# Kernel tuning notes

Hardware: AMD Instinct MI355X
Metric: run time of the kernel (lower is better)

The kernel has to match this reference:

```python
import jax, jax.numpy as jnp
import numpy as np

N = 100000   # total nodes
E = 1000000  # edges
D = 64       # input_dim
H = 128      # embed_dim


def setup_inputs() -> dict:
    key = jax.random.key(0)
    k1, k2, k3, k4 = jax.random.split(key, 4)
    nodes = jnp.arange(N, dtype=jnp.int32)
    features = jax.random.normal(k1, (N, D), dtype=jnp.float32)
    edge_index = jax.random.randint(k2, (2, E), 0, N, dtype=jnp.int32)
    # nn.Linear(2*D, H): weight [H, 2D], bias [H]
    W = jax.random.normal(k3, (H, 2 * D), dtype=jnp.float32) / np.sqrt(2 * D)
    b = jax.random.normal(k4, (H,), dtype=jnp.float32) * 0.01
    return {"nodes": nodes, "features": features, "edge_index": edge_index,
            "W": W, "b": b}


def reference(nodes, features, edge_index, W, b):
    src, dst = edge_index[0], edge_index[1]
    # gcn=False: neighbors are undirected (both src->dst and dst->src).
    # Mean aggregator over all neighbors (full-neighborhood mean).
    ones = jnp.ones((E,), dtype=features.dtype)
    neigh_sum = (jax.ops.segment_sum(features[dst], src, num_segments=N)
                 + jax.ops.segment_sum(features[src], dst, num_segments=N))
    deg = (jax.ops.segment_sum(ones, src, num_segments=N)
           + jax.ops.segment_sum(ones, dst, num_segments=N))
    neigh_mean = neigh_sum / jnp.maximum(deg, 1.0)[:, None]  # [N, D]
    self_feats = features[nodes]            # [B, D]
    neigh_feats = neigh_mean[nodes]         # [B, D]
    combined = jnp.concatenate([self_feats, neigh_feats], axis=1)  # [B, 2D]
    out = jax.nn.relu(combined @ W.T + b)   # [B, H]
    return out
```

## Files before the change

### kernel.cpp

```cpp
#include <hip/hip_runtime.h>
#include <hip/hip_bf16.h>


#define D_IN 64
#define H_OUT 128
#define CAP 64
#define CAP_L 61
#define NPB 32
#define BSHIFT 8
#define BUK_N 256
#define NBUK_MAX 512
#define PASSA_BLOCKS 256
#define PASSA_THREADS 512

typedef unsigned long long ull;
typedef unsigned short ushortt;
typedef unsigned char uchar;
typedef __attribute__((ext_vector_type(8))) short bf16x8;
typedef __attribute__((ext_vector_type(4))) float f32x4;
typedef __attribute__((ext_vector_type(2))) float f32x2;

__device__ __forceinline__ ushortt f2bf(float f) {
    __hip_bfloat16 h = __float2bfloat16(f);
    return *reinterpret_cast<ushortt*>(&h);
}
__device__ __forceinline__ float bf2f(ushortt u) {
    unsigned int x = ((unsigned int)u) << 16;
    return __uint_as_float(x);
}

__global__ __launch_bounds__(PASSA_THREADS) void prep_kernel(
    const int* __restrict__ ei,
    unsigned* __restrict__ gbuf,
    int* __restrict__ blkcnt,
    const float4* __restrict__ feat4,
    const float4* __restrict__ w4,
    ushortt* __restrict__ fb,
    uint2* __restrict__ fq,
    ushortt* __restrict__ Wb,
    int E, int nbuk, int scap, int chunk, int nfeat8, int nw8)
{
    const int t = threadIdx.x;

    if (blockIdx.x >= PASSA_BLOCKS) {
        int i = (blockIdx.x - PASSA_BLOCKS) * PASSA_THREADS + t;
        if (i < nfeat8) {
            float4 a = feat4[2 * i], b = feat4[2 * i + 1];
            bf16x8 o;
            o[0] = (short)f2bf(a.x); o[1] = (short)f2bf(a.y);
            o[2] = (short)f2bf(a.z); o[3] = (short)f2bf(a.w);
            o[4] = (short)f2bf(b.x); o[5] = (short)f2bf(b.y);
            o[6] = (short)f2bf(b.z); o[7] = (short)f2bf(b.w);
            *(bf16x8*)&fb[(size_t)i * 8] = o;
            unsigned lo = (unsigned)__builtin_amdgcn_cvt_pk_fp8_f32(a.x, a.y, 0, false);
            lo = (unsigned)__builtin_amdgcn_cvt_pk_fp8_f32(a.z, a.w, (int)lo, true);
            unsigned hi = (unsigned)__builtin_amdgcn_cvt_pk_fp8_f32(b.x, b.y, 0, false);
            hi = (unsigned)__builtin_amdgcn_cvt_pk_fp8_f32(b.z, b.w, (int)hi, true);
            uint2 q; q.x = lo; q.y = hi;
            fq[i] = q;
        } else {
            int j = i - nfeat8;
            if (j < nw8) {
                float4 a = w4[2 * j], b = w4[2 * j + 1];
                bf16x8 o;
                o[0] = (short)f2bf(a.x); o[1] = (short)f2bf(a.y);
                o[2] = (short)f2bf(a.z); o[3] = (short)f2bf(a.w);
                o[4] = (short)f2bf(b.x); o[5] = (short)f2bf(b.y);
                o[6] = (short)f2bf(b.z); o[7] = (short)f2bf(b.w);
                *(bf16x8*)&Wb[(size_t)j * 8] = o;
            }
        }
        return;
    }

    __shared__ int lcnt[NBUK_MAX];
    for (int i = t; i < nbuk; i += PASSA_THREADS) lcnt[i] = 0;
    __syncthreads();

    const int E2 = 2 * E;
    int lo = blockIdx.x * chunk;
    int hi = lo + chunk; if (hi > E2) hi = E2;

    for (int i = lo + t; i < hi; i += PASSA_THREADS) {
        int u = ei[i];
        int v = (i < E) ? ei[E + i] : ei[i - E];
        int b = u >> BSHIFT;
        unsigned pk = ((unsigned)v << BSHIFT) | (unsigned)(u & (BUK_N - 1));
        int p = atomicAdd(&lcnt[b], 1);
        if (p < scap) gbuf[((size_t)blockIdx.x * nbuk + b) * scap + p] = pk;
    }
    __syncthreads();
    for (int b = t; b < nbuk; b += PASSA_THREADS)
        blkcnt[blockIdx.x * nbuk + b] = lcnt[b];
}

__global__ __launch_bounds__(1024) void adj_agg_kernel(
    const unsigned* __restrict__ gbuf,
    const int* __restrict__ blkcnt,
    const int* __restrict__ ei,
    const uchar* __restrict__ fq,
    ushortt* __restrict__ meanb,
    int N, int E, int nbuk, int scap)
{
    __shared__ unsigned adj_l[BUK_N * CAP_L];
    __shared__ int cnt_l[BUK_N];
    __shared__ int scnt_l[PASSA_BLOCKS];
    __shared__ int satf;

    const int b = blockIdx.x;
    const int t = threadIdx.x;

    if (t == 0) satf = 0;
    if (t < BUK_N) cnt_l[t] = 0;
    if (t < PASSA_BLOCKS) {
        int c = blkcnt[t * nbuk + b];
        scnt_l[t] = c;
        if (c > scap) satf = 1;
    }
    __syncthreads();

    const int wv   = t >> 6;
    const int lane = t & 63;

    if (satf) {
        const int E2 = 2 * E;
        for (int i = t; i < E2; i += 1024) {
            int u = ei[i];
            if ((u >> BSHIFT) != b) continue;
            int v = (i < E) ? ei[E + i] : ei[i - E];
            int ul = u & (BUK_N - 1);
            int p  = atomicAdd(&cnt_l[ul], 1);
            if (p < CAP_L) adj_l[ul * CAP_L + p] = (unsigned)v;
        }
    } else {
        for (int seg = wv; seg < PASSA_BLOCKS; seg += 16) {
            int c = scnt_l[seg]; if (c > scap) c = scap;
            const unsigned* base = gbuf + ((size_t)seg * nbuk + b) * scap;
            for (int i = lane; i < c; i += 64) {
                unsigned e = base[i];
                int ul = e & (BUK_N - 1);
                int v  = (int)(e >> BSHIFT);
                int p  = atomicAdd(&cnt_l[ul], 1);
                if (p < CAP_L) adj_l[ul * CAP_L + p] = (unsigned)v;
            }
        }
    }
    __syncthreads();

    const int oct = lane >> 3;
    const int ol  = lane & 7;
    const uchar* fqb = fq + ol * 8;

    const int nbase = wv * 16;
    const int gbase = (b << BSHIFT) + nbase;

#define GATH(U0, U1, U2, U3, AROW, CC)                                       \
    {                                                                        \
        if ((CC) > 0) {                                                      \
            int jj = oct;      int a = jj < (CC);                            \
            unsigned id = (AROW)[a ? jj : 0];                                \
            U0 = *(const uint2*)(fqb + (size_t)(id * 64u));                  \
            if (!a) { U0.x = 0u; U0.y = 0u; }                                \
        }                                                                    \
        if ((CC) > 8) {                                                      \
            int jj = 8 + oct;  int a = jj < (CC);                            \
            unsigned id = (AROW)[a ? jj : 0];                                \
            U1 = *(const uint2*)(fqb + (size_t)(id * 64u));                  \
            if (!a) { U1.x = 0u; U1.y = 0u; }                                \
        }                                                                    \
        if ((CC) > 16) {                                                     \
            int jj = 16 + oct; int a = jj < (CC);                            \
            unsigned id = (AROW)[a ? jj : 0];                                \
            U2 = *(const uint2*)(fqb + (size_t)(id * 64u));                  \
            if (!a) { U2.x = 0u; U2.y = 0u; }                                \
        }                                                                    \
        if ((CC) > 24) {                                                     \
            int jj = 24 + oct; int a = jj < (CC);                            \
            unsigned id = (AROW)[a ? jj : 0];                                \
            U3 = *(const uint2*)(fqb + (size_t)(id * 64u));                  \
            if (!a) { U3.x = 0u; U3.y = 0u; }                                \
        }                                                                    \
    }

#define DEC(u)                                                       \
    s0 += __builtin_amdgcn_cvt_pk_f32_fp8((int)(u).x, false);        \
    s1 += __builtin_amdgcn_cvt_pk_f32_fp8((int)(u).x, true);         \
    s2 += __builtin_amdgcn_cvt_pk_f32_fp8((int)(u).y, false);        \
    s3 += __builtin_amdgcn_cvt_pk_f32_fp8((int)(u).y, true);

#define FINISH(UA, UB, UC, UD, CC, CTRUE, AROW, G)                           \
    {                                                                        \
        f32x2 s0 = {0.f, 0.f}, s1 = {0.f, 0.f};                              \
        f32x2 s2 = {0.f, 0.f}, s3 = {0.f, 0.f};                              \
        DEC(UA); DEC(UB); DEC(UC); DEC(UD);                                  \
        if (__builtin_expect((CC) > 32, 0)) {                                \
            for (int j = 32; j < (CC); j += 8) {                             \
                int jj = j + oct; int a = jj < (CC);                         \
                unsigned id = (AROW)[a ? jj : 0];                            \
                uint2 u = *(const uint2*)(fqb + (size_t)(id * 64u));         \
                if (!a) { u.x = 0u; u.y = 0u; }                              \
                DEC(u);                                                      \
            }                                                                \
        }                                                                    \
        f32x2 a0, a1;                                                        \
        {                                                                    \
            f32x2 t0, t1, t2, t3;                                            \
            t0.x = __shfl_xor(s0.x, 8);  t0.y = __shfl_xor(s0.y, 8);         \
            t1.x = __shfl_xor(s1.x, 8);  t1.y = __shfl_xor(s1.y, 8);         \
            t2.x = __shfl_xor(s2.x, 8);  t2.y = __shfl_xor(s2.y, 8);         \
            t3.x = __shfl_xor(s3.x, 8);  t3.y = __shfl_xor(s3.y, 8);         \
            bool hi = (oct & 1);                                             \
            a0 = hi ? (s2 + t2) : (s0 + t0);                                 \
            a1 = hi ? (s3 + t3) : (s1 + t1);                                 \
        }                                                                    \
        f32x2 b0;                                                            \
        {                                                                    \
            f32x2 t0, t1;                                                    \
            t0.x = __shfl_xor(a0.x, 16); t0.y = __shfl_xor(a0.y, 16);        \
            t1.x = __shfl_xor(a1.x, 16); t1.y = __shfl_xor(a1.y, 16);        \
            bool hi = (oct & 2);                                             \
            b0 = hi ? (a1 + t1) : (a0 + t0);                                 \
        }                                                                    \
        float cf;                                                            \
        {                                                                    \
            f32x2 tt;                                                        \
            tt.x = __shfl_xor(b0.x, 32); tt.y = __shfl_xor(b0.y, 32);        \
            f32x2 ss = b0 + tt;                                              \
            cf = (oct & 4) ? ss.y : ss.x;                                    \
        }                                                                    \
        float r = 1.0f / fmaxf((float)(CTRUE), 1.0f);                        \
        int d = 8 * ol + 4 * (oct & 1) + (oct & 2) + ((oct >> 2) & 1);       \
        meanb[(size_t)(G) * D_IN + d] = f2bf(cf * r);                        \
    }

    for (int np = 0; np < 8; ++np) {
        const int n0 = nbase + 2 * np;
        const int g0 = gbase + 2 * np;
        const int g1 = g0 + 1;

        const int c0  = (g0 < N) ? cnt_l[n0] : 0;
        const int c1  = (g1 < N) ? cnt_l[n0 + 1] : 0;
        const int cc0 = c0 < CAP_L ? c0 : CAP_L;
        const int cc1 = c1 < CAP_L ? c1 : CAP_L;
        const unsigned* ar0 = &adj_l[n0 * CAP_L];
        const unsigned* ar1 = &adj_l[(n0 + 1) * CAP_L];

        uint2 u00 = {0u,0u}, u01 = {0u,0u}, u02 = {0u,0u}, u03 = {0u,0u};
        uint2 u10 = {0u,0u}, u11 = {0u,0u}, u12 = {0u,0u}, u13 = {0u,0u};
        GATH(u00, u01, u02, u03, ar0, cc0);
        GATH(u10, u11, u12, u13, ar1, cc1);

        if (g0 < N) FINISH(u00, u01, u02, u03, cc0, c0, ar0, g0);
        if (g1 < N) FINISH(u10, u11, u12, u13, cc1, c1, ar1, g1);
    }
#undef GATH
#undef DEC
#undef FINISH
}

__global__ __launch_bounds__(256) void build_adj_kernel(
    const int* __restrict__ ei,
    int* __restrict__ cnt,
    int* __restrict__ adj,
    int E)
{
    const int part   = blockIdx.x & 7;
    const int bloc   = blockIdx.x >> 3;
    const int nbp    = gridDim.x >> 3;
    const int stride = nbp * 256;
    const int E2     = 2 * E;

    for (int i = bloc * 256 + (int)threadIdx.x; i < E2; i += stride) {
        int u = ei[i];
        if (((u >> 4) & 7) != part) continue;
        int v = (i < E) ? ei[E + i] : ei[i - E];
        int p = atomicAdd(&cnt[u], 1);
        if (p < CAP_L) adj[u * CAP + p] = v;
    }
}

__global__ __launch_bounds__(256) void aggregate_f32_kernel(
    const float* __restrict__ feat,
    const int* __restrict__ adj,
    const int* __restrict__ cnt,
    ushortt* __restrict__ meanb,
    int N)
{
    int wid  = (blockIdx.x * blockDim.x + threadIdx.x) >> 6;
    int lane = threadIdx.x & 63;
    if (wid >= N) return;

    int c  = cnt[wid];
    int cc = c < CAP_L ? c : CAP_L;
    int ids = adj[wid * CAP + lane];

    float sum = 0.0f;
    int j = 0;
    for (; j + 8 <= cc; j += 8) {
        int i0 = __shfl(ids, j + 0);
        int i1 = __shfl(ids, j + 1);
        int i2 = __shfl(ids, j + 2);
        int i3 = __shfl(ids, j + 3);
        int i4 = __shfl(ids, j + 4);
        int i5 = __shfl(ids, j + 5);
        int i6 = __shfl(ids, j + 6);
        int i7 = __shfl(ids, j + 7);
        float f0 = feat[i0 * D_IN + lane];
        float f1 = feat[i1 * D_IN + lane];
        float f2 = feat[i2 * D_IN + lane];
        float f3 = feat[i3 * D_IN + lane];
        float f4 = feat[i4 * D_IN + lane];
        float f5 = feat[i5 * D_IN + lane];
        float f6 = feat[i6 * D_IN + lane];
        float f7 = feat[i7 * D_IN + lane];
        sum += ((f0 + f1) + (f2 + f3)) + ((f4 + f5) + (f6 + f7));
    }
    for (; j < cc; ++j)
        sum += feat[__shfl(ids, j) * D_IN + lane];

    float m = sum / fmaxf((float)c, 1.0f);
    meanb[(size_t)wid * D_IN + lane] = f2bf(m);
}

__global__ __launch_bounds__(256) void gemm_mfma_kernel(
    const int* __restrict__ nodes,
    const ushortt* __restrict__ fb,
    const ushortt* __restrict__ meanb,
    const ushortt* __restrict__ Wb,
    const float* __restrict__ bias,
    float* __restrict__ out,
    int N)
{
    __shared__ ushortt w_lds[128 * 136];
    __shared__ int gnode[64];

    const int t  = threadIdx.x;
    const int n0 = blockIdx.x * 64;

    if (t < 64) {
        int idx = n0 + t;
        gnode[t] = nodes[idx < N ? idx : N - 1];
    }
    for (int i = t; i < 128 * 16; i += 256) {
        int row = i >> 4, seg = i & 15;
        *(bf16x8*)&w_lds[row * 136 + seg * 8] =
            *(const bf16x8*)&Wb[row * 128 + seg * 8];
    }
    __syncthreads();

    const int w    = t >> 6;
    const int lane = t & 63;
    const int l15  = lane & 15;
    const int quad = lane >> 4;

    const int g = gnode[w * 16 + l15];
    const bf16x8 a0 = *(const bf16x8*)&fb[(size_t)g * D_IN +  0 + quad * 8];
    const bf16x8 a1 = *(const bf16x8*)&fb[(size_t)g * D_IN + 32 + quad * 8];
    const bf16x8 a2 = *(const bf16x8*)&meanb[(size_t)g * D_IN +  0 + quad * 8];
    const bf16x8 a3 = *(const bf16x8*)&meanb[(size_t)g * D_IN + 32 + quad * 8];

    const int  out_row = n0 + w * 16 + l15;
    const bool valid   = out_row < N;

#pragma unroll
    for (int tile = 0; tile < 8; ++tile) {
        const int h0 = tile * 16;
        const ushortt* wrow = &w_lds[(h0 + l15) * 136];
        bf16x8 b0 = *(const bf16x8*)&wrow[ 0 + quad * 8];
        bf16x8 b1 = *(const bf16x8*)&wrow[32 + quad * 8];
        bf16x8 b2 = *(const bf16x8*)&wrow[64 + quad * 8];
        bf16x8 b3 = *(const bf16x8*)&wrow[96 + quad * 8];

        f32x4 acc = {0.f, 0.f, 0.f, 0.f};
        acc = __builtin_amdgcn_mfma_f32_16x16x32_bf16(b0, a0, acc, 0, 0, 0);
        acc = __builtin_amdgcn_mfma_f32_16x16x32_bf16(b1, a1, acc, 0, 0, 0);
        acc = __builtin_amdgcn_mfma_f32_16x16x32_bf16(b2, a2, acc, 0, 0, 0);
        acc = __builtin_amdgcn_mfma_f32_16x16x32_bf16(b3, a3, acc, 0, 0, 0);

        if (valid) {
            float4 bv = *(const float4*)&bias[h0 + quad * 4];
            float4 o;
            o.x = fmaxf(acc[0] + bv.x, 0.0f);
            o.y = fmaxf(acc[1] + bv.y, 0.0f);
            o.z = fmaxf(acc[2] + bv.z, 0.0f);
            o.w = fmaxf(acc[3] + bv.w, 0.0f);
            *(float4*)&out[(size_t)out_row * H_OUT + h0 + quad * 4] = o;
        }
    }
}

__global__ __launch_bounds__(256) void gemm_kernel(
    const int* __restrict__ nodes,
    const float* __restrict__ feat,
    const ushortt* __restrict__ meanb,
    const float* __restrict__ W,
    const float* __restrict__ bias,
    float* __restrict__ out,
    int N)
{
    __shared__ float w_lds[64 * 132];
    __shared__ float comb_self[NPB * 68];
    __shared__ float comb_mean[NPB * 68];
    __shared__ int   gnode[NPB];

    const int t  = threadIdx.x;
    const int n0 = blockIdx.x * NPB;

    if (t < NPB) {
        int idx = n0 + t;
        if (idx >= N) idx = N - 1;
        gnode[t] = nodes[idx];
    }
    __syncthreads();

    for (int i = t; i < NPB * 64; i += 256) {
        int n = i >> 6, d = i & 63;
        int g = gnode[n];
        comb_self[n * 68 + d] = feat[g * D_IN + d];
        comb_mean[n * 68 + d] = bf2f(meanb[(size_t)g * D_IN + d]);
    }
    for (int i = t; i < H_OUT * 64; i += 256) {
        int h = i >> 6, kk = i & 63;
        w_lds[kk * 132 + h] = W[h * (2 * D_IN) + kk];
    }
    __syncthreads();

    const int tx = t & 31;
    const int ty = t >> 5;
    const int h0 = tx * 4;
    const int nl = ty * 4;

    float acc[4][4];
#pragma unroll
    for (int j = 0; j < 4; j++)
#pragma unroll
        for (int i = 0; i < 4; i++) acc[j][i] = 0.0f;

    for (int kk = 0; kk < 64; kk += 4) {
        float4 wvv[4], cv[4];
#pragma unroll
        for (int i = 0; i < 4; i++)
            wvv[i] = *(const float4*)&w_lds[(kk + i) * 132 + h0];
#pragma unroll
        for (int j = 0; j < 4; j++)
            cv[j] = *(const float4*)&comb_self[(nl + j) * 68 + kk];
#pragma unroll
        for (int j = 0; j < 4; j++) {
            const float* c = (const float*)&cv[j];
#pragma unroll
            for (int i = 0; i < 4; i++) {
                const float* wp = (const float*)&wvv[i];
                acc[j][0] += wp[0] * c[i];
                acc[j][1] += wp[1] * c[i];
                acc[j][2] += wp[2] * c[i];
                acc[j][3] += wp[3] * c[i];
            }
        }
    }
    __syncthreads();

    for (int i = t; i < H_OUT * 64; i += 256) {
        int h = i >> 6, kk = i & 63;
        w_lds[kk * 132 + h] = W[h * (2 * D_IN) + 64 + kk];
    }
    __syncthreads();

    for (int kk = 0; kk < 64; kk += 4) {
        float4 wvv[4], cv[4];
#pragma unroll
        for (int i = 0; i < 4; i++)
            wvv[i] = *(const float4*)&w_lds[(kk + i) * 132 + h0];
#pragma unroll
        for (int j = 0; j < 4; j++)
            cv[j] = *(const float4*)&comb_mean[(nl + j) * 68 + kk];
#pragma unroll
        for (int j = 0; j < 4; j++) {
            const float* c = (const float*)&cv[j];
#pragma unroll
            for (int i = 0; i < 4; i++) {
                const float* wp = (const float*)&wvv[i];
                acc[j][0] += wp[0] * c[i];
                acc[j][1] += wp[1] * c[i];
                acc[j][2] += wp[2] * c[i];
                acc[j][3] += wp[3] * c[i];
            }
        }
    }

    float4 bv = *(const float4*)&bias[h0];
#pragma unroll
    for (int j = 0; j < 4; j++) {
        int n = n0 + nl + j;
        if (n >= N) continue;
        float4 o;
        o.x = fmaxf(acc[j][0] + bv.x, 0.0f);
        o.y = fmaxf(acc[j][1] + bv.y, 0.0f);
        o.z = fmaxf(acc[j][2] + bv.z, 0.0f);
        o.w = fmaxf(acc[j][3] + bv.w, 0.0f);
        *(float4*)&out[(size_t)n * H_OUT + h0] = o;
    }
}

extern "C" void kernel_launch(void* const* d_in, const int* in_sizes, int n_in,
                              void* d_out, int out_size, void* d_ws, size_t ws_size,
                              hipStream_t stream) {
    const int*   nodes = (const int*)d_in[0];
    const float* feat  = (const float*)d_in[1];
    const int*   ei    = (const int*)d_in[2];
    const float* W     = (const float*)d_in[3];
    const float* bias  = (const float*)d_in[4];
    float*       out   = (float*)d_out;

    const int N  = in_sizes[0];
    const int E  = in_sizes[2] / 2;
    const int E2 = 2 * E;

    const int nbuk  = (N + BUK_N - 1) >> BSHIFT;
    const int chunk = (E2 + PASSA_BLOCKS - 1) / PASSA_BLOCKS;
    double ex = (double)chunk * (double)BUK_N / (double)N;
    int scap = ((int)(ex + 9.0 * __builtin_sqrt(ex)) + 31) & ~15;
    if (scap < 64) scap = 64;

    char* base = (char*)d_ws;
    size_t off = 0;
    auto aln = [](size_t x) { return (x + 63) & ~(size_t)63; };
    int*     cnt    = (int*)(base + off);     off = aln(off + (size_t)N * 4);
    int*     adj    = (int*)(base + off);     off = aln(off + (size_t)N * CAP * 4);
    ushortt* meanb  = (ushortt*)(base + off); off = aln(off + (size_t)N * D_IN * 2);
    int*     blkcnt = (int*)(base + off);     off = aln(off + (size_t)PASSA_BLOCKS * NBUK_MAX * 4);
    ushortt* Wb     = (ushortt*)(base + off); off = aln(off + (size_t)H_OUT * 2 * D_IN * 2);
    ushortt* fb     = (ushortt*)(base + off); off = aln(off + (size_t)N * D_IN * 2);
    uchar*   fq     = (uchar*)(base + off);   off = aln(off + (size_t)N * D_IN);
    unsigned* gbuf  = (unsigned*)(base + off);
    const size_t total = off + (size_t)PASSA_BLOCKS * nbuk * scap * 4;

    const bool full = (N <= 131072) && (nbuk <= NBUK_MAX) && (ws_size >= total)
                   && ((N * D_IN) % 8 == 0);

    if (full) {
        const int nfeat8 = N * D_IN / 8;
        const int nw8    = H_OUT * 2 * D_IN / 8;
        const int conv_blocks = (nfeat8 + nw8 + PASSA_THREADS - 1) / PASSA_THREADS;
        prep_kernel<<<PASSA_BLOCKS + conv_blocks, PASSA_THREADS, 0, stream>>>(
            ei, gbuf, blkcnt, (const float4*)feat, (const float4*)W,
            fb, (uint2*)fq, Wb, E, nbuk, scap, chunk, nfeat8, nw8);
        adj_agg_kernel<<<nbuk, 1024, 0, stream>>>(gbuf, blkcnt, ei, fq,
                                                  meanb, N, E, nbuk, scap);
        gemm_mfma_kernel<<<(N + 63) / 64, 256, 0, stream>>>(
            nodes, fb, meanb, Wb, bias, out, N);
    } else {
        const int ablocks = (int)(((size_t)N * 64 + 255) / 256);
        hipMemsetAsync(cnt, 0, (size_t)N * sizeof(int), stream);
        build_adj_kernel<<<2048, 256, 0, stream>>>(ei, cnt, adj, E);
        aggregate_f32_kernel<<<ablocks, 256, 0, stream>>>(feat, adj, cnt,
                                                          meanb, N);
        gemm_kernel<<<(N + NPB - 1) / NPB, 256, 0, stream>>>(
            nodes, feat, meanb, W, bias, out, N);
    }
}
```

Measured before the change: 169.9 us.

## Fuse prep, aggregation and GEMM into one cooperative kernel with grid syncs

Replaces the three-kernel pipeline (edge bucketing plus conversion, adjacency aggregation, MFMA GEMM) with a single cooperative mega-kernel launched with one 1024-thread block per bucket. Grid-wide syncs separate the phases, which removes the launch gaps between kernels and lets the bucketing use nbuk segments instead of a fixed 256. The original kernels remain as a fallback when a cooperative launch is not possible. The trade-off is grid.sync cost, a 1024-thread block size for the conversion and GEMM phases, and occupancy limits from the large shared buffer.

New measurement: 175.6 us. 1.03x slower.

```diff
diff --git a/kernel.cpp b/kernel.cpp
--- a/kernel.cpp
+++ b/kernel.cpp
@@ -1,5 +1,6 @@
 #include <hip/hip_runtime.h>
 #include <hip/hip_bf16.h>
+#include <hip/hip_cooperative_groups.h>
 
 
 #define D_IN 64
@@ -10,8 +11,11 @@
 #define BSHIFT 8
 #define BUK_N 256
 #define NBUK_MAX 512
+#define NSEG_MAX 448
 #define PASSA_BLOCKS 256
 #define PASSA_THREADS 512
+
+namespace cg = cooperative_groups;
 
 typedef unsigned long long ull;
 typedef unsigned short ushortt;
@@ -29,155 +33,30 @@
     return __uint_as_float(x);
 }
 
-__global__ __launch_bounds__(PASSA_THREADS) void prep_kernel(
-    const int* __restrict__ ei,
-    unsigned* __restrict__ gbuf,
-    int* __restrict__ blkcnt,
-    const float4* __restrict__ feat4,
-    const float4* __restrict__ w4,
-    ushortt* __restrict__ fb,
-    uint2* __restrict__ fq,
-    ushortt* __restrict__ Wb,
-    int E, int nbuk, int scap, int chunk, int nfeat8, int nw8)
-{
-    const int t = threadIdx.x;
-
-    if (blockIdx.x >= PASSA_BLOCKS) {
-        int i = (blockIdx.x - PASSA_BLOCKS) * PASSA_THREADS + t;
-        if (i < nfeat8) {
-            float4 a = feat4[2 * i], b = feat4[2 * i + 1];
-            bf16x8 o;
-            o[0] = (short)f2bf(a.x); o[1] = (short)f2bf(a.y);
-            o[2] = (short)f2bf(a.z); o[3] = (short)f2bf(a.w);
-            o[4] = (short)f2bf(b.x); o[5] = (short)f2bf(b.y);
-            o[6] = (short)f2bf(b.z); o[7] = (short)f2bf(b.w);
-            *(bf16x8*)&fb[(size_t)i * 8] = o;
-            unsigned lo = (unsigned)__builtin_amdgcn_cvt_pk_fp8_f32(a.x, a.y, 0, false);
-            lo = (unsigned)__builtin_amdgcn_cvt_pk_fp8_f32(a.z, a.w, (int)lo, true);
-            unsigned hi = (unsigned)__builtin_amdgcn_cvt_pk_fp8_f32(b.x, b.y, 0, false);
-            hi = (unsigned)__builtin_amdgcn_cvt_pk_fp8_f32(b.z, b.w, (int)hi, true);
-            uint2 q; q.x = lo; q.y = hi;
-            fq[i] = q;
-        } else {
-            int j = i - nfeat8;
-            if (j < nw8) {
-                float4 a = w4[2 * j], b = w4[2 * j + 1];
-                bf16x8 o;
-                o[0] = (short)f2bf(a.x); o[1] = (short)f2bf(a.y);
-                o[2] = (short)f2bf(a.z); o[3] = (short)f2bf(a.w);
-                o[4] = (short)f2bf(b.x); o[5] = (short)f2bf(b.y);
-                o[6] = (short)f2bf(b.z); o[7] = (short)f2bf(b.w);
-                *(bf16x8*)&Wb[(size_t)j * 8] = o;
-            }
-        }
-        return;
-    }
-
-    __shared__ int lcnt[NBUK_MAX];
-    for (int i = t; i < nbuk; i += PASSA_THREADS) lcnt[i] = 0;
-    __syncthreads();
-
-    const int E2 = 2 * E;
-    int lo = blockIdx.x * chunk;
-    int hi = lo + chunk; if (hi > E2) hi = E2;
-
-    for (int i = lo + t; i < hi; i += PASSA_THREADS) {
-        int u = ei[i];
-        int v = (i < E) ? ei[E + i] : ei[i - E];
-        int b = u >> BSHIFT;
-        unsigned pk = ((unsigned)v << BSHIFT) | (unsigned)(u & (BUK_N - 1));
-        int p = atomicAdd(&lcnt[b], 1);
-        if (p < scap) gbuf[((size_t)blockIdx.x * nbuk + b) * scap + p] = pk;
-    }
-    __syncthreads();
-    for (int b = t; b < nbuk; b += PASSA_THREADS)
-        blkcnt[blockIdx.x * nbuk + b] = lcnt[b];
-}
-
-__global__ __launch_bounds__(1024) void adj_agg_kernel(
-    const unsigned* __restrict__ gbuf,
-    const int* __restrict__ blkcnt,
-    const int* __restrict__ ei,
-    const uchar* __restrict__ fq,
-    ushortt* __restrict__ meanb,
-    int N, int E, int nbuk, int scap)
-{
-    __shared__ unsigned adj_l[BUK_N * CAP_L];
-    __shared__ int cnt_l[BUK_N];
-    __shared__ int scnt_l[PASSA_BLOCKS];
-    __shared__ int satf;
-
-    const int b = blockIdx.x;
-    const int t = threadIdx.x;
-
-    if (t == 0) satf = 0;
-    if (t < BUK_N) cnt_l[t] = 0;
-    if (t < PASSA_BLOCKS) {
-        int c = blkcnt[t * nbuk + b];
-        scnt_l[t] = c;
-        if (c > scap) satf = 1;
-    }
-    __syncthreads();
-
-    const int wv   = t >> 6;
-    const int lane = t & 63;
-
-    if (satf) {
-        const int E2 = 2 * E;
-        for (int i = t; i < E2; i += 1024) {
-            int u = ei[i];
-            if ((u >> BSHIFT) != b) continue;
-            int v = (i < E) ? ei[E + i] : ei[i - E];
-            int ul = u & (BUK_N - 1);
-            int p  = atomicAdd(&cnt_l[ul], 1);
-            if (p < CAP_L) adj_l[ul * CAP_L + p] = (unsigned)v;
-        }
-    } else {
-        for (int seg = wv; seg < PASSA_BLOCKS; seg += 16) {
-            int c = scnt_l[seg]; if (c > scap) c = scap;
-            const unsigned* base = gbuf + ((size_t)seg * nbuk + b) * scap;
-            for (int i = lane; i < c; i += 64) {
-                unsigned e = base[i];
-                int ul = e & (BUK_N - 1);
-                int v  = (int)(e >> BSHIFT);
-                int p  = atomicAdd(&cnt_l[ul], 1);
-                if (p < CAP_L) adj_l[ul * CAP_L + p] = (unsigned)v;
-            }
-        }
-    }
-    __syncthreads();
-
-    const int oct = lane >> 3;
-    const int ol  = lane & 7;
-    const uchar* fqb = fq + ol * 8;
-
-    const int nbase = wv * 16;
-    const int gbase = (b << BSHIFT) + nbase;
-
-#define GATH(U0, U1, U2, U3, AROW, CC)                                       \
+#define GATH(U0, U1, U2, U3, AROW, CC, FQB)                                  \
     {                                                                        \
         if ((CC) > 0) {                                                      \
             int jj = oct;      int a = jj < (CC);                            \
             unsigned id = (AROW)[a ? jj : 0];                                \
-            U0 = *(const uint2*)(fqb + (size_t)(id * 64u));                  \
+            U0 = *(const uint2*)((FQB) + (size_t)(id * 64u));                \
             if (!a) { U0.x = 0u; U0.y = 0u; }                                \
         }                                                                    \
         if ((CC) > 8) {                                                      \
             int jj = 8 + oct;  int a = jj < (CC);                            \
             unsigned id = (AROW)[a ? jj : 0];                                \
-            U1 = *(const uint2*)(fqb + (size_t)(id * 64u));                  \
+            U1 = *(const uint2*)((FQB) + (size_t)(id * 64u));                \
             if (!a) { U1.x = 0u; U1.y = 0u; }                                \
         }                                                                    \
         if ((CC) > 16) {                                                     \
             int jj = 16 + oct; int a = jj < (CC);                            \
             unsigned id = (AROW)[a ? jj : 0];                                \
-            U2 = *(const uint2*)(fqb + (size_t)(id * 64u));                  \
+            U2 = *(const uint2*)((FQB) + (size_t)(id * 64u));                \
             if (!a) { U2.x = 0u; U2.y = 0u; }                                \
         }                                                                    \
         if ((CC) > 24) {                                                     \
             int jj = 24 + oct; int a = jj < (CC);                            \
             unsigned id = (AROW)[a ? jj : 0];                                \
-            U3 = *(const uint2*)(fqb + (size_t)(id * 64u));                  \
+            U3 = *(const uint2*)((FQB) + (size_t)(id * 64u));                \
             if (!a) { U3.x = 0u; U3.y = 0u; }                                \
         }                                                                    \
     }
@@ -188,7 +67,7 @@
     s2 += __builtin_amdgcn_cvt_pk_f32_fp8((int)(u).y, false);        \
     s3 += __builtin_amdgcn_cvt_pk_f32_fp8((int)(u).y, true);
 
-#define FINISH(UA, UB, UC, UD, CC, CTRUE, AROW, G)                           \
+#define FINISH(UA, UB, UC, UD, CC, CTRUE, AROW, G, FQB, MEANB)               \
     {                                                                        \
         f32x2 s0 = {0.f, 0.f}, s1 = {0.f, 0.f};                              \
         f32x2 s2 = {0.f, 0.f}, s3 = {0.f, 0.f};                              \
@@ -197,7 +76,7 @@
             for (int j = 32; j < (CC); j += 8) {                             \
                 int jj = j + oct; int a = jj < (CC);                         \
                 unsigned id = (AROW)[a ? jj : 0];                            \
-                uint2 u = *(const uint2*)(fqb + (size_t)(id * 64u));         \
+                uint2 u = *(const uint2*)((FQB) + (size_t)(id * 64u));       \
                 if (!a) { u.x = 0u; u.y = 0u; }                              \
                 DEC(u);                                                      \
             }                                                                \
@@ -230,8 +109,340 @@
         }                                                                    \
         float r = 1.0f / fmaxf((float)(CTRUE), 1.0f);                        \
         int d = 8 * ol + 4 * (oct & 1) + (oct & 2) + ((oct >> 2) & 1);       \
-        meanb[(size_t)(G) * D_IN + d] = f2bf(cf * r);                        \
-    }
+        (MEANB)[(size_t)(G) * D_IN + d] = f2bf(cf * r);                      \
+    }
+
+#define SMEM_BYTES 65296
+
+__global__ __launch_bounds__(1024, 8) void mega_kernel(
+    const int* __restrict__ ei,
+    unsigned* __restrict__ gbuf,
+    int* __restrict__ blkcnt,
+    const float4* __restrict__ feat4,
+    const float4* __restrict__ w4,
+    ushortt* __restrict__ fb,
+    uint2* __restrict__ fq,
+    ushortt* __restrict__ Wb,
+    ushortt* __restrict__ meanb,
+    const int* __restrict__ nodes,
+    const float* __restrict__ bias,
+    float* __restrict__ out,
+    int N, int E, int nbuk, int scap, int chunk, int nfeat8, int nw8)
+{
+    cg::grid_group grid = cg::this_grid();
+    __shared__ __attribute__((aligned(16))) char smem[SMEM_BYTES];
+
+    const int b = blockIdx.x;
+    const int t = threadIdx.x;
+    const int E2 = 2 * E;
+
+    {
+        int* lcnt = (int*)smem;
+        for (int i = t; i < nbuk; i += 1024) lcnt[i] = 0;
+        __syncthreads();
+
+        int lo = b * chunk;
+        int hi = lo + chunk; if (hi > E2) hi = E2;
+        for (int i = lo + t; i < hi; i += 1024) {
+            int u = ei[i];
+            int v = (i < E) ? ei[E + i] : ei[i - E];
+            int bk = u >> BSHIFT;
+            unsigned pk = ((unsigned)v << BSHIFT) | (unsigned)(u & (BUK_N - 1));
+            int p = atomicAdd(&lcnt[bk], 1);
+            if (p < scap) gbuf[((size_t)b * nbuk + bk) * scap + p] = pk;
+        }
+        __syncthreads();
+        for (int i = t; i < nbuk; i += 1024)
+            blkcnt[b * nbuk + i] = lcnt[i];
+
+        const int total = nfeat8 + nw8;
+        for (int i = b * 1024 + t; i < total; i += gridDim.x * 1024) {
+            if (i < nfeat8) {
+                float4 a = feat4[2 * i], bb = feat4[2 * i + 1];
+                bf16x8 o;
+                o[0] = (short)f2bf(a.x);  o[1] = (short)f2bf(a.y);
+                o[2] = (short)f2bf(a.z);  o[3] = (short)f2bf(a.w);
+                o[4] = (short)f2bf(bb.x); o[5] = (short)f2bf(bb.y);
+                o[6] = (short)f2bf(bb.z); o[7] = (short)f2bf(bb.w);
+                *(bf16x8*)&fb[(size_t)i * 8] = o;
+                unsigned lo8 = (unsigned)__builtin_amdgcn_cvt_pk_fp8_f32(a.x, a.y, 0, false);
+                lo8 = (unsigned)__builtin_amdgcn_cvt_pk_fp8_f32(a.z, a.w, (int)lo8, true);
+                unsigned hi8 = (unsigned)__builtin_amdgcn_cvt_pk_fp8_f32(bb.x, bb.y, 0, false);
+                hi8 = (unsigned)__builtin_amdgcn_cvt_pk_fp8_f32(bb.z, bb.w, (int)hi8, true);
+                uint2 q; q.x = lo8; q.y = hi8;
+                fq[i] = q;
+            } else {
+                int j = i - nfeat8;
+                float4 a = w4[2 * j], bb = w4[2 * j + 1];
+                bf16x8 o;
+                o[0] = (short)f2bf(a.x);  o[1] = (short)f2bf(a.y);
+                o[2] = (short)f2bf(a.z);  o[3] = (short)f2bf(a.w);
+                o[4] = (short)f2bf(bb.x); o[5] = (short)f2bf(bb.y);
+                o[6] = (short)f2bf(bb.z); o[7] = (short)f2bf(bb.w);
+                *(bf16x8*)&Wb[(size_t)j * 8] = o;
+            }
+        }
+    }
+    __threadfence();
+    grid.sync();
+
+    {
+        unsigned* adj_l  = (unsigned*)smem;
+        int*      cnt_l  = (int*)(smem + 62464);
+        int*      scnt_l = (int*)(smem + 63488);
+        int*      satf   = (int*)(smem + 65280);
+
+        const int nseg = gridDim.x;
+        if (t == 0) *satf = 0;
+        if (t < BUK_N) cnt_l[t] = 0;
+        for (int s = t; s < nseg; s += 1024) {
+            int c = blkcnt[s * nbuk + b];
+            scnt_l[s] = c;
+            if (c > scap) *satf = 1;
+        }
+        __syncthreads();
+
+        const int wv   = t >> 6;
+        const int lane = t & 63;
+
+        if (*satf) {
+            for (int i = t; i < E2; i += 1024) {
+                int u = ei[i];
+                if ((u >> BSHIFT) != b) continue;
+                int v = (i < E) ? ei[E + i] : ei[i - E];
+                int ul = u & (BUK_N - 1);
+                int p  = atomicAdd(&cnt_l[ul], 1);
+                if (p < CAP_L) adj_l[ul * CAP_L + p] = (unsigned)v;
+            }
+        } else {
+            for (int seg = wv; seg < nseg; seg += 16) {
+                int c = scnt_l[seg]; if (c > scap) c = scap;
+                const unsigned* base = gbuf + ((size_t)seg * nbuk + b) * scap;
+                for (int i = lane; i < c; i += 64) {
+                    unsigned e = base[i];
+                    int ul = e & (BUK_N - 1);
+                    int v  = (int)(e >> BSHIFT);
+                    int p  = atomicAdd(&cnt_l[ul], 1);
+                    if (p < CAP_L) adj_l[ul * CAP_L + p] = (unsigned)v;
+                }
+            }
+        }
+        __syncthreads();
+
+        const int oct = lane >> 3;
+        const int ol  = lane & 7;
+        const uchar* fqb = (const uchar*)fq + ol * 8;
+        const int nbase = wv * 16;
+        const int gbase = (b << BSHIFT) + nbase;
+
+        for (int np = 0; np < 8; ++np) {
+            const int n0 = nbase + 2 * np;
+            const int g0 = gbase + 2 * np;
+            const int g1 = g0 + 1;
+
+            const int c0  = (g0 < N) ? cnt_l[n0] : 0;
+            const int c1  = (g1 < N) ? cnt_l[n0 + 1] : 0;
+            const int cc0 = c0 < CAP_L ? c0 : CAP_L;
+            const int cc1 = c1 < CAP_L ? c1 : CAP_L;
+            const unsigned* ar0 = &adj_l[n0 * CAP_L];
+            const unsigned* ar1 = &adj_l[(n0 + 1) * CAP_L];
+
+            uint2 u00 = {0u,0u}, u01 = {0u,0u}, u02 = {0u,0u}, u03 = {0u,0u};
+            uint2 u10 = {0u,0u}, u11 = {0u,0u}, u12 = {0u,0u}, u13 = {0u,0u};
+            GATH(u00, u01, u02, u03, ar0, cc0, fqb);
+            GATH(u10, u11, u12, u13, ar1, cc1, fqb);
+
+            if (g0 < N) FINISH(u00, u01, u02, u03, cc0, c0, ar0, g0, fqb, meanb);
+            if (g1 < N) FINISH(u10, u11, u12, u13, cc1, c1, ar1, g1, fqb, meanb);
+        }
+    }
+    __threadfence();
+    grid.sync();
+
+    {
+        ushortt* w_lds = (ushortt*)smem;
+        for (int i = t; i < 128 * 16; i += 1024) {
+            int row = i >> 4, seg = i & 15;
+            *(bf16x8*)&w_lds[row * 136 + seg * 8] =
+                *(const bf16x8*)&Wb[row * 128 + seg * 8];
+        }
+        __syncthreads();
+
+        const int grp  = t >> 8;
+        const int t256 = t & 255;
+        const int w    = t256 >> 6;
+        const int lane = t256 & 63;
+        const int l15  = lane & 15;
+        const int quad = lane >> 4;
+
+        const int ntiles = (N + 63) >> 6;
+        for (int tile_id = b * 4 + grp; tile_id < ntiles;
+             tile_id += gridDim.x * 4) {
+            const int n0 = tile_id * 64;
+            int idx = n0 + w * 16 + l15;
+            const int g = nodes[idx < N ? idx : N - 1];
+
+            const bf16x8 a0 = *(const bf16x8*)&fb[(size_t)g * D_IN +  0 + quad * 8];
+            const bf16x8 a1 = *(const bf16x8*)&fb[(size_t)g * D_IN + 32 + quad * 8];
+            const bf16x8 a2 = *(const bf16x8*)&meanb[(size_t)g * D_IN +  0 + quad * 8];
+            const bf16x8 a3 = *(const bf16x8*)&meanb[(size_t)g * D_IN + 32 + quad * 8];
+
+            const int  out_row = n0 + w * 16 + l15;
+            const bool valid   = out_row < N;
+
+#pragma unroll
+            for (int tile = 0; tile < 8; ++tile) {
+                const int h0 = tile * 16;
+                const ushortt* wrow = &w_lds[(h0 + l15) * 136];
+                bf16x8 b0 = *(const bf16x8*)&wrow[ 0 + quad * 8];
+                bf16x8 b1 = *(const bf16x8*)&wrow[32 + quad * 8];
+                bf16x8 b2 = *(const bf16x8*)&wrow[64 + quad * 8];
+                bf16x8 b3 = *(const bf16x8*)&wrow[96 + quad * 8];
+
+                f32x4 acc = {0.f, 0.f, 0.f, 0.f};
+                acc = __builtin_amdgcn_mfma_f32_16x16x32_bf16(b0, a0, acc, 0, 0, 0);
+                acc = __builtin_amdgcn_mfma_f32_16x16x32_bf16(b1, a1, acc, 0, 0, 0);
+                acc = __builtin_amdgcn_mfma_f32_16x16x32_bf16(b2, a2, acc, 0, 0, 0);
+                acc = __builtin_amdgcn_mfma_f32_16x16x32_bf16(b3, a3, acc, 0, 0, 0);
+
+                if (valid) {
+                    float4 bv = *(const float4*)&bias[h0 + quad * 4];
+                    float4 o;
+                    o.x = fmaxf(acc[0] + bv.x, 0.0f);
+                    o.y = fmaxf(acc[1] + bv.y, 0.0f);
+                    o.z = fmaxf(acc[2] + bv.z, 0.0f);
+                    o.w = fmaxf(acc[3] + bv.w, 0.0f);
+                    *(float4*)&out[(size_t)out_row * H_OUT + h0 + quad * 4] = o;
+                }
+            }
+        }
+    }
+}
+
+
+__global__ __launch_bounds__(PASSA_THREADS) void prep_kernel(
+    const int* __restrict__ ei,
+    unsigned* __restrict__ gbuf,
+    int* __restrict__ blkcnt,
+    const float4* __restrict__ feat4,
+    const float4* __restrict__ w4,
+    ushortt* __restrict__ fb,
+    uint2* __restrict__ fq,
+    ushortt* __restrict__ Wb,
+    int E, int nbuk, int scap, int chunk, int nfeat8, int nw8)
+{
+    const int t = threadIdx.x;
+
+    if (blockIdx.x >= PASSA_BLOCKS) {
+        int i = (blockIdx.x - PASSA_BLOCKS) * PASSA_THREADS + t;
+        if (i < nfeat8) {
+            float4 a = feat4[2 * i], b = feat4[2 * i + 1];
+            bf16x8 o;
+            o[0] = (short)f2bf(a.x); o[1] = (short)f2bf(a.y);
+            o[2] = (short)f2bf(a.z); o[3] = (short)f2bf(a.w);
+            o[4] = (short)f2bf(b.x); o[5] = (short)f2bf(b.y);
+            o[6] = (short)f2bf(b.z); o[7] = (short)f2bf(b.w);
+            *(bf16x8*)&fb[(size_t)i * 8] = o;
+            unsigned lo = (unsigned)__builtin_amdgcn_cvt_pk_fp8_f32(a.x, a.y, 0, false);
+            lo = (unsigned)__builtin_amdgcn_cvt_pk_fp8_f32(a.z, a.w, (int)lo, true);
+            unsigned hi = (unsigned)__builtin_amdgcn_cvt_pk_fp8_f32(b.x, b.y, 0, false);
+            hi = (unsigned)__builtin_amdgcn_cvt_pk_fp8_f32(b.z, b.w, (int)hi, true);
+            uint2 q; q.x = lo; q.y = hi;
+            fq[i] = q;
+        } else {
+            int j = i - nfeat8;
+            if (j < nw8) {
+                float4 a = w4[2 * j], b = w4[2 * j + 1];
+                bf16x8 o;
+                o[0] = (short)f2bf(a.x); o[1] = (short)f2bf(a.y);
+                o[2] = (short)f2bf(a.z); o[3] = (short)f2bf(a.w);
+                o[4] = (short)f2bf(b.x); o[5] = (short)f2bf(b.y);
+                o[6] = (short)f2bf(b.z); o[7] = (short)f2bf(b.w);
+                *(bf16x8*)&Wb[(size_t)j * 8] = o;
+            }
+        }
+        return;
+    }
+
+    __shared__ int lcnt[NBUK_MAX];
+    for (int i = t; i < nbuk; i += PASSA_THREADS) lcnt[i] = 0;
+    __syncthreads();
+
+    const int E2 = 2 * E;
+    int lo = blockIdx.x * chunk;
+    int hi = lo + chunk; if (hi > E2) hi = E2;
+
+    for (int i = lo + t; i < hi; i += PASSA_THREADS) {
+        int u = ei[i];
+        int v = (i < E) ? ei[E + i] : ei[i - E];
+        int b = u >> BSHIFT;
+        unsigned pk = ((unsigned)v << BSHIFT) | (unsigned)(u & (BUK_N - 1));
+        int p = atomicAdd(&lcnt[b], 1);
+        if (p < scap) gbuf[((size_t)blockIdx.x * nbuk + b) * scap + p] = pk;
+    }
+    __syncthreads();
+    for (int b = t; b < nbuk; b += PASSA_THREADS)
+        blkcnt[blockIdx.x * nbuk + b] = lcnt[b];
+}
+
+__global__ __launch_bounds__(1024) void adj_agg_kernel(
+    const unsigned* __restrict__ gbuf,
+    const int* __restrict__ blkcnt,
+    const int* __restrict__ ei,
+    const uchar* __restrict__ fqc,
+    ushortt* __restrict__ meanb,
+    int N, int E, int nbuk, int scap)
+{
+    __shared__ unsigned adj_l[BUK_N * CAP_L];
+    __shared__ int cnt_l[BUK_N];
+    __shared__ int scnt_l[PASSA_BLOCKS];
+    __shared__ int satf;
+
+    const int b = blockIdx.x;
+    const int t = threadIdx.x;
+
+    if (t == 0) satf = 0;
+    if (t < BUK_N) cnt_l[t] = 0;
+    if (t < PASSA_BLOCKS) {
+        int c = blkcnt[t * nbuk + b];
+        scnt_l[t] = c;
+        if (c > scap) satf = 1;
+    }
+    __syncthreads();
+
+    const int wv   = t >> 6;
+    const int lane = t & 63;
+
+    if (satf) {
+        const int E2 = 2 * E;
+        for (int i = t; i < E2; i += 1024) {
+            int u = ei[i];
+            if ((u >> BSHIFT) != b) continue;
+            int v = (i < E) ? ei[E + i] : ei[i - E];
+            int ul = u & (BUK_N - 1);
+            int p  = atomicAdd(&cnt_l[ul], 1);
+            if (p < CAP_L) adj_l[ul * CAP_L + p] = (unsigned)v;
+        }
+    } else {
+        for (int seg = wv; seg < PASSA_BLOCKS; seg += 16) {
+            int c = scnt_l[seg]; if (c > scap) c = scap;
+            const unsigned* base = gbuf + ((size_t)seg * nbuk + b) * scap;
+            for (int i = lane; i < c; i += 64) {
+                unsigned e = base[i];
+                int ul = e & (BUK_N - 1);
+                int v  = (int)(e >> BSHIFT);
+                int p  = atomicAdd(&cnt_l[ul], 1);
+                if (p < CAP_L) adj_l[ul * CAP_L + p] = (unsigned)v;
+            }
+        }
+    }
+    __syncthreads();
+
+    const int oct = lane >> 3;
+    const int ol  = lane & 7;
+    const uchar* fqb = fqc + ol * 8;
+    const int nbase = wv * 16;
+    const int gbase = (b << BSHIFT) + nbase;
 
     for (int np = 0; np < 8; ++np) {
         const int n0 = nbase + 2 * np;
@@ -247,15 +458,79 @@
 
         uint2 u00 = {0u,0u}, u01 = {0u,0u}, u02 = {0u,0u}, u03 = {0u,0u};
         uint2 u10 = {0u,0u}, u11 = {0u,0u}, u12 = {0u,0u}, u13 = {0u,0u};
-        GATH(u00, u01, u02, u03, ar0, cc0);
-        GATH(u10, u11, u12, u13, ar1, cc1);
-
-        if (g0 < N) FINISH(u00, u01, u02, u03, cc0, c0, ar0, g0);
-        if (g1 < N) FINISH(u10, u11, u12, u13, cc1, c1, ar1, g1);
-    }
-#undef GATH
-#undef DEC
-#undef FINISH
+        GATH(u00, u01, u02, u03, ar0, cc0, fqb);
+        GATH(u10, u11, u12, u13, ar1, cc1, fqb);
+
+        if (g0 < N) FINISH(u00, u01, u02, u03, cc0, c0, ar0, g0, fqb, meanb);
+        if (g1 < N) FINISH(u10, u11, u12, u13, cc1, c1, ar1, g1, fqb, meanb);
+    }
+}
+
+__global__ __launch_bounds__(256) void gemm_mfma_kernel(
+    const int* __restrict__ nodes,
+    const ushortt* __restrict__ fb,
+    const ushortt* __restrict__ meanb,
+    const ushortt* __restrict__ Wb,
+    const float* __restrict__ bias,
+    float* __restrict__ out,
+    int N)
+{
+    __shared__ ushortt w_lds[128 * 136];
+    __shared__ int gnode[64];
+
+    const int t  = threadIdx.x;
+    const int n0 = blockIdx.x * 64;
+
+    if (t < 64) {
+        int idx = n0 + t;
+        gnode[t] = nodes[idx < N ? idx : N - 1];
+    }
+    for (int i = t; i < 128 * 16; i += 256) {
+        int row = i >> 4, seg = i & 15;
+        *(bf16x8*)&w_lds[row * 136 + seg * 8] =
+            *(const bf16x8*)&Wb[row * 128 + seg * 8];
+    }
+    __syncthreads();
+
+    const int w    = t >> 6;
+    const int lane = t & 63;
+    const int l15  = lane & 15;
+    const int quad = lane >> 4;
+
+    const int g = gnode[w * 16 + l15];
+    const bf16x8 a0 = *(const bf16x8*)&fb[(size_t)g * D_IN +  0 + quad * 8];
+    const bf16x8 a1 = *(const bf16x8*)&fb[(size_t)g * D_IN + 32 + quad * 8];
+    const bf16x8 a2 = *(const bf16x8*)&meanb[(size_t)g * D_IN +  0 + quad * 8];
+    const bf16x8 a3 = *(const bf16x8*)&meanb[(size_t)g * D_IN + 32 + quad * 8];
+
+    const int  out_row = n0 + w * 16 + l15;
+    const bool valid   = out_row < N;
+
+#pragma unroll
+    for (int tile = 0; tile < 8; ++tile) {
+        const int h0 = tile * 16;
+        const ushortt* wrow = &w_lds[(h0 + l15) * 136];
+        bf16x8 b0 = *(const bf16x8*)&wrow[ 0 + quad * 8];
+        bf16x8 b1 = *(const bf16x8*)&wrow[32 + quad * 8];
+        bf16x8 b2 = *(const bf16x8*)&wrow[64 + quad * 8];
+        bf16x8 b3 = *(const bf16x8*)&wrow[96 + quad * 8];
+
+        f32x4 acc = {0.f, 0.f, 0.f, 0.f};
+        acc = __builtin_amdgcn_mfma_f32_16x16x32_bf16(b0, a0, acc, 0, 0, 0);
+        acc = __builtin_amdgcn_mfma_f32_16x16x32_bf16(b1, a1, acc, 0, 0, 0);
+        acc = __builtin_amdgcn_mfma_f32_16x16x32_bf16(b2, a2, acc, 0, 0, 0);
+        acc = __builtin_amdgcn_mfma_f32_16x16x32_bf16(b3, a3, acc, 0, 0, 0);
+
+        if (valid) {
+            float4 bv = *(const float4*)&bias[h0 + quad * 4];
+            float4 o;
+            o.x = fmaxf(acc[0] + bv.x, 0.0f);
+            o.y = fmaxf(acc[1] + bv.y, 0.0f);
+            o.z = fmaxf(acc[2] + bv.z, 0.0f);
+            o.w = fmaxf(acc[3] + bv.w, 0.0f);
+            *(float4*)&out[(size_t)out_row * H_OUT + h0 + quad * 4] = o;
+        }
+    }
 }
 
 __global__ __launch_bounds__(256) void build_adj_kernel(
@@ -322,73 +597,6 @@
     meanb[(size_t)wid * D_IN + lane] = f2bf(m);
 }
 
-__global__ __launch_bounds__(256) void gemm_mfma_kernel(
-    const int* __restrict__ nodes,
-    const ushortt* __restrict__ fb,
-    const ushortt* __restrict__ meanb,
-    const ushortt* __restrict__ Wb,
-    const float* __restrict__ bias,
-    float* __restrict__ out,
-    int N)
-{
-    __shared__ ushortt w_lds[128 * 136];
-    __shared__ int gnode[64];
-
-    const int t  = threadIdx.x;
-    const int n0 = blockIdx.x * 64;
-
-    if (t < 64) {
-        int idx = n0 + t;
-        gnode[t] = nodes[idx < N ? idx : N - 1];
-    }
-    for (int i = t; i < 128 * 16; i += 256) {
-        int row = i >> 4, seg = i & 15;
-        *(bf16x8*)&w_lds[row * 136 + seg * 8] =
-            *(const bf16x8*)&Wb[row * 128 + seg * 8];
-    }
-    __syncthreads();
-
-    const int w    = t >> 6;
-    const int lane = t & 63;
-    const int l15  = lane & 15;
-    const int quad = lane >> 4;
-
-    const int g = gnode[w * 16 + l15];
-    const bf16x8 a0 = *(const bf16x8*)&fb[(size_t)g * D_IN +  0 + quad * 8];
-    const bf16x8 a1 = *(const bf16x8*)&fb[(size_t)g * D_IN + 32 + quad * 8];
-    const bf16x8 a2 = *(const bf16x8*)&meanb[(size_t)g * D_IN +  0 + quad * 8];
-    const bf16x8 a3 = *(const bf16x8*)&meanb[(size_t)g * D_IN + 32 + quad * 8];
-
-    const int  out_row = n0 + w * 16 + l15;
-    const bool valid   = out_row < N;
-
-#pragma unroll
-    for (int tile = 0; tile < 8; ++tile) {
-        const int h0 = tile * 16;
-        const ushortt* wrow = &w_lds[(h0 + l15) * 136];
-        bf16x8 b0 = *(const bf16x8*)&wrow[ 0 + quad * 8];
-        bf16x8 b1 = *(const bf16x8*)&wrow[32 + quad * 8];
-        bf16x8 b2 = *(const bf16x8*)&wrow[64 + quad * 8];
-        bf16x8 b3 = *(const bf16x8*)&wrow[96 + quad * 8];
-
-        f32x4 acc = {0.f, 0.f, 0.f, 0.f};
-        acc = __builtin_amdgcn_mfma_f32_16x16x32_bf16(b0, a0, acc, 0, 0, 0);
-        acc = __builtin_amdgcn_mfma_f32_16x16x32_bf16(b1, a1, acc, 0, 0, 0);
-        acc = __builtin_amdgcn_mfma_f32_16x16x32_bf16(b2, a2, acc, 0, 0, 0);
-        acc = __builtin_amdgcn_mfma_f32_16x16x32_bf16(b3, a3, acc, 0, 0, 0);
-
-        if (valid) {
-            float4 bv = *(const float4*)&bias[h0 + quad * 4];
-            float4 o;
-            o.x = fmaxf(acc[0] + bv.x, 0.0f);
-            o.y = fmaxf(acc[1] + bv.y, 0.0f);
-            o.z = fmaxf(acc[2] + bv.z, 0.0f);
-            o.w = fmaxf(acc[3] + bv.w, 0.0f);
-            *(float4*)&out[(size_t)out_row * H_OUT + h0 + quad * 4] = o;
-        }
-    }
-}
-
 __global__ __launch_bounds__(256) void gemm_kernel(
     const int* __restrict__ nodes,
     const float* __restrict__ feat,
@@ -515,11 +723,17 @@
     const int E  = in_sizes[2] / 2;
     const int E2 = 2 * E;
 
-    const int nbuk  = (N + BUK_N - 1) >> BSHIFT;
-    const int chunk = (E2 + PASSA_BLOCKS - 1) / PASSA_BLOCKS;
-    double ex = (double)chunk * (double)BUK_N / (double)N;
-    int scap = ((int)(ex + 9.0 * __builtin_sqrt(ex)) + 31) & ~15;
-    if (scap < 64) scap = 64;
+    const int nbuk = (N + BUK_N - 1) >> BSHIFT;
+
+    const int chunkC = (E2 + nbuk - 1) / nbuk;
+    double exC = (double)chunkC * (double)BUK_N / (double)N;
+    int scapC = ((int)(exC + 9.0 * __builtin_sqrt(exC)) + 31) & ~15;
+    if (scapC < 64) scapC = 64;
+
+    const int chunkP = (E2 + PASSA_BLOCKS - 1) / PASSA_BLOCKS;
+    double exP = (double)chunkP * (double)BUK_N / (double)N;
+    int scapP = ((int)(exP + 9.0 * __builtin_sqrt(exP)) + 31) & ~15;
+    if (scapP < 64) scapP = 64;
 
     char* base = (char*)d_ws;
     size_t off = 0;
@@ -527,25 +741,55 @@
     int*     cnt    = (int*)(base + off);     off = aln(off + (size_t)N * 4);
     int*     adj    = (int*)(base + off);     off = aln(off + (size_t)N * CAP * 4);
     ushortt* meanb  = (ushortt*)(base + off); off = aln(off + (size_t)N * D_IN * 2);
-    int*     blkcnt = (int*)(base + off);     off = aln(off + (size_t)PASSA_BLOCKS * NBUK_MAX * 4);
+    int*     blkcnt = (int*)(base + off);     off = aln(off + (size_t)NSEG_MAX * NBUK_MAX * 4);
     ushortt* Wb     = (ushortt*)(base + off); off = aln(off + (size_t)H_OUT * 2 * D_IN * 2);
     ushortt* fb     = (ushortt*)(base + off); off = aln(off + (size_t)N * D_IN * 2);
     uchar*   fq     = (uchar*)(base + off);   off = aln(off + (size_t)N * D_IN);
     unsigned* gbuf  = (unsigned*)(base + off);
-    const size_t total = off + (size_t)PASSA_BLOCKS * nbuk * scap * 4;
-
-    const bool full = (N <= 131072) && (nbuk <= NBUK_MAX) && (ws_size >= total)
-                   && ((N * D_IN) % 8 == 0);
-
-    if (full) {
-        const int nfeat8 = N * D_IN / 8;
-        const int nw8    = H_OUT * 2 * D_IN / 8;
-        const int conv_blocks = (nfeat8 + nw8 + PASSA_THREADS - 1) / PASSA_THREADS;
+
+    const size_t coop_total    = off + (size_t)nbuk * nbuk * scapC * 4;
+    const size_t noncoop_total = off + (size_t)PASSA_BLOCKS * nbuk * scapP * 4;
+
+    const bool base_ok = (N <= 114688) && ((N * D_IN) % 8 == 0);
+    const int nfeat8 = N * D_IN / 8;
+    const int nw8    = H_OUT * 2 * D_IN / 8;
+
+    int coop_ok = 0;
+    if (base_ok && nbuk >= 1 && nbuk <= NSEG_MAX && ws_size >= coop_total) {
+        int dev = 0;
+        if (hipGetDevice(&dev) == hipSuccess) {
+            int ncu = 0, maxb = 0;
+            if (hipDeviceGetAttribute(&ncu, hipDeviceAttributeMultiprocessorCount,
+                                      dev) == hipSuccess &&
+                hipOccupancyMaxActiveBlocksPerMultiprocessor(
+                    &maxb, (const void*)mega_kernel, 1024, 0) == hipSuccess) {
+                if ((long long)maxb * ncu >= nbuk) coop_ok = 1;
+            }
+        }
+    }
+
+    if (coop_ok) {
+        const float4* feat4 = (const float4*)feat;
+        const float4* w4    = (const float4*)W;
+        uint2* fq2 = (uint2*)fq;
+        int N_ = N, E_ = E, nbuk_ = nbuk, scap_ = scapC, chunk_ = chunkC;
+        int nf8_ = nfeat8, nw8_ = nw8;
+        void* args[] = {
+            (void*)&ei, (void*)&gbuf, (void*)&blkcnt, (void*)&feat4,
+            (void*)&w4, (void*)&fb, (void*)&fq2, (void*)&Wb, (void*)&meanb,
+            (void*)&nodes, (void*)&bias, (void*)&out,
+            (void*)&N_, (void*)&E_, (void*)&nbuk_, (void*)&scap_,
+            (void*)&chunk_, (void*)&nf8_, (void*)&nw8_ };
+        hipLaunchCooperativeKernel(reinterpret_cast<void*>(mega_kernel),
+                                   dim3(nbuk), dim3(1024), args, 0, stream);
+    } else if (base_ok && nbuk <= NBUK_MAX && ws_size >= noncoop_total) {
+        const int conv_blocks =
+            (nfeat8 + nw8 + PASSA_THREADS - 1) / PASSA_THREADS;
         prep_kernel<<<PASSA_BLOCKS + conv_blocks, PASSA_THREADS, 0, stream>>>(
             ei, gbuf, blkcnt, (const float4*)feat, (const float4*)W,
-            fb, (uint2*)fq, Wb, E, nbuk, scap, chunk, nfeat8, nw8);
+            fb, (uint2*)fq, Wb, E, nbuk, scapP, chunkP, nfeat8, nw8);
         adj_agg_kernel<<<nbuk, 1024, 0, stream>>>(gbuf, blkcnt, ei, fq,
-                                                  meanb, N, E, nbuk, scap);
+                                                  meanb, N, E, nbuk, scapP);
         gemm_mfma_kernel<<<(N + 63) / 64, 256, 0, stream>>>(
             nodes, fb, meanb, Wb, bias, out, N);
     } else {
```
